# Optimization experiments

Measured on AMD Instinct MI355X. Metric: run time of the kernel, lower is better.

The kernel has to match this reference:

```python
import jax, jax.numpy as jnp
import numpy as np

B, C, S = 32768, 30, 7
COORD, NOOBJ = 5.0, 0.5


def setup_inputs() -> dict:
    key = jax.random.key(0)
    k1, k2, k3 = jax.random.split(key, 3)
    # uniform in [0.05, 1): size loss takes sqrt of raw channels, so keep them positive
    pre = jax.random.uniform(k1, (B, C, S, S), jnp.float32, 0.05, 1.0)
    lab = jax.random.uniform(k2, (B, C, S, S), jnp.float32, 0.05, 1.0)
    # channel 4 of the label is a binary objectness indicator (code tests == 1)
    objm = (jax.random.uniform(k3, (B, S, S)) < 0.3).astype(jnp.float32)
    lab = lab.at[:, 4].set(objm)
    return {"pre": pre, "lab": lab}


def _iou(b1, b2):
    # b1, b2: [B, 4, S, S] with channels (x1, y1, x2, y2); original '+1' pixel convention
    ix1 = jnp.maximum(b1[:, 0], b2[:, 0])
    iy1 = jnp.maximum(b1[:, 1], b2[:, 1])
    ix2 = jnp.minimum(b1[:, 2], b2[:, 2])
    iy2 = jnp.minimum(b1[:, 3], b2[:, 3])
    inter = jnp.maximum(ix2 - ix1 + 1.0, 0.0) * jnp.maximum(iy2 - iy1 + 1.0, 0.0)
    a1 = (b1[:, 2] - b1[:, 0] + 1.0) * (b1[:, 3] - b1[:, 1] + 1.0)
    a2 = (b2[:, 2] - b2[:, 0] + 1.0) * (b2[:, 3] - b2[:, 1] + 1.0)
    return inter / (a1 + a2 - inter)


def reference(pre, lab):
    obj = lab[:, 4] == 1.0                      # [B,S,S] objectness mask
    iou1 = _iou(pre[:, 0:4], lab[:, 0:4])       # box 1 IoU
    iou2 = _iou(pre[:, 5:9], lab[:, 5:9])       # box 2 IoU
    resp1 = iou1 >= iou2                        # box 1 responsible

    # coordinate loss: the px*64 / py*64 grid offsets cancel in (cxl - cxp)
    addr1 = COORD * ((lab[:, 0] - pre[:, 0]) ** 2 + (lab[:, 1] - pre[:, 1]) ** 2)
    addr2 = COORD * ((lab[:, 5] - pre[:, 5]) ** 2 + (lab[:, 6] - pre[:, 6]) ** 2)

    size1 = COORD * ((jnp.sqrt(pre[:, 2]) - jnp.sqrt(lab[:, 2])) ** 2
                     + (jnp.sqrt(pre[:, 3]) - jnp.sqrt(lab[:, 3])) ** 2)
    size2 = COORD * ((jnp.sqrt(pre[:, 7]) - jnp.sqrt(lab[:, 7])) ** 2
                     + (jnp.sqrt(pre[:, 8]) - jnp.sqrt(lab[:, 8])) ** 2)

    # original always uses pre[9] as the responsible confidence (faithful to source)
    conf = NOOBJ * (pre[:, 9] - jnp.where(resp1, iou1, iou2)) ** 2

    obj_terms = jnp.where(resp1, addr1 + size1, addr2 + size2) + conf
    noobj_terms = NOOBJ * (pre[:, 4] + pre[:, 9]) ** 2

    # class loss is accumulated for every cell regardless of objectness
    cls = jnp.sum((pre[:, 10:] - lab[:, 10:]) ** 2)

    total = jnp.sum(jnp.where(obj, obj_terms, noobj_terms)) + cls
    return total / B
```

## Files before the change

kernel.cpp:

```cpp
#include <hip/hip_runtime.h>


#define BATCH   32768
#define S2      49
#define CPB     1470
#define NB      2
#define GF      (NB * CPB)
#define GV      (GF / 4)
#define NGROUPS (BATCH / NB)
#define LDSB    492
#define HALF    (NB * LDSB)
#define BUFSZ   (2 * HALF)
#define NBLK    2048

__device__ __forceinline__ float iou4(float px1, float py1, float px2, float py2,
                                      float lx1, float ly1, float lx2, float ly2) {
    float ix1 = fmaxf(px1, lx1), iy1 = fmaxf(py1, ly1);
    float ix2 = fminf(px2, lx2), iy2 = fminf(py2, ly2);
    float iw = fmaxf(ix2 - ix1 + 1.0f, 0.0f);
    float ih = fmaxf(iy2 - iy1 + 1.0f, 0.0f);
    float inter = iw * ih;
    float a1 = (px2 - px1 + 1.0f) * (py2 - py1 + 1.0f);
    float a2 = (lx2 - lx1 + 1.0f) * (ly2 - ly1 + 1.0f);
    return inter / (a1 + a2 - inter);
}

__device__ __forceinline__ float cell_loss(const float* P, const float* L) {
    float p0 = P[0],   p1 = P[49],  p2 = P[98],  p3 = P[147], p4 = P[196];
    float p5 = P[245], p6 = P[294], p7 = P[343], p8 = P[392], p9 = P[441];
    float l0 = L[0],   l1 = L[49],  l2 = L[98],  l3 = L[147], l4 = L[196];
    float l5 = L[245], l6 = L[294], l7 = L[343], l8 = L[392];

    float iou1 = iou4(p0, p1, p2, p3, l0, l1, l2, l3);
    float iou2 = iou4(p5, p6, p7, p8, l5, l6, l7, l8);
    bool resp1 = iou1 >= iou2;

    float d0 = l0 - p0, d1 = l1 - p1, d5 = l5 - p5, d6 = l6 - p6;
    float addr1 = 5.0f * (d0 * d0 + d1 * d1);
    float addr2 = 5.0f * (d5 * d5 + d6 * d6);

    float e2 = sqrtf(p2) - sqrtf(l2), e3 = sqrtf(p3) - sqrtf(l3);
    float e7 = sqrtf(p7) - sqrtf(l7), e8 = sqrtf(p8) - sqrtf(l8);
    float size1 = 5.0f * (e2 * e2 + e3 * e3);
    float size2 = 5.0f * (e7 * e7 + e8 * e8);

    float du = p9 - (resp1 ? iou1 : iou2);
    float conf = 0.5f * du * du;

    float obj_terms = (resp1 ? (addr1 + size1) : (addr2 + size2)) + conf;
    float pn = p4 + p9;
    float noobj = 0.5f * pn * pn;
    return (l4 == 1.0f) ? obj_terms : noobj;
}

__device__ __forceinline__ void consume_one(float4 pv, float4 lv, int i,
                                            float* __restrict__ buf, float& acc) {
    int base = 4 * i;
    int bl = base >= CPB;
    int lo = base - bl * CPB;
    if (lo <= 486) {
        *(float4*)(buf + bl * LDSB + lo) = pv;
        *(float4*)(buf + HALF + bl * LDSB + lo) = lv;
    } else if (lo >= 490 && lo <= 1466) {
        float d0 = pv.x - lv.x, d1 = pv.y - lv.y;
        float d2 = pv.z - lv.z, d3 = pv.w - lv.w;
        acc += d0 * d0 + d1 * d1 + d2 * d2 + d3 * d3;
    } else if (lo == 488) {
        buf[bl * LDSB + 488] = pv.x;
        buf[bl * LDSB + 489] = pv.y;
        buf[HALF + bl * LDSB + 488] = lv.x;
        buf[HALF + bl * LDSB + 489] = lv.y;
        float d2 = pv.z - lv.z, d3 = pv.w - lv.w;
        acc += d2 * d2 + d3 * d3;
    } else {
        float d0 = pv.x - lv.x, d1 = pv.y - lv.y;
        acc += d0 * d0 + d1 * d1;
        buf[LDSB + 0] = pv.z;
        buf[LDSB + 1] = pv.w;
        buf[HALF + LDSB + 0] = lv.z;
        buf[HALF + LDSB + 1] = lv.w;
    }
}

__global__ __launch_bounds__(256) void yolo_loss_main(const float4* __restrict__ pre4,
                                                      const float4* __restrict__ lab4,
                                                      float* __restrict__ partials) {
    __shared__ __align__(16) float sbuf[2 * BUFSZ];
    __shared__ float red[4];
    const int tid = threadIdx.x;
    const bool t2 = tid + 512 < GV;
    float acc = 0.0f;

    float* cb   = sbuf;
    float* nbuf = sbuf + BUFSZ;

    int g = blockIdx.x;
    {
        const float4* __restrict__ ps = pre4 + (size_t)g * GV;
        const float4* __restrict__ ls = lab4 + (size_t)g * GV;
        float4 pa = ps[tid];
        float4 la = ls[tid];
        float4 pb = ps[tid + 256];
        float4 lb = ls[tid + 256];
        float4 pc, lc;
        if (t2) { pc = ps[tid + 512]; lc = ls[tid + 512]; }
        consume_one(pa, la, tid,       cb, acc);
        consume_one(pb, lb, tid + 256, cb, acc);
        if (t2) consume_one(pc, lc, tid + 512, cb, acc);
    }
    __syncthreads();

    for (;;) {
        int gn = g + gridDim.x;
        bool hn = gn < NGROUPS;
        float4 pa, la, pb, lb, pc, lc;
        if (hn) {
            const float4* __restrict__ ps = pre4 + (size_t)gn * GV;
            const float4* __restrict__ ls = lab4 + (size_t)gn * GV;
            pa = ps[tid];
            la = ls[tid];
            pb = ps[tid + 256];
            lb = ls[tid + 256];
            if (t2) { pc = ps[tid + 512]; lc = ls[tid + 512]; }
        }
        if (tid < NB * S2) {
            int bl = tid / S2, s = tid - bl * S2;
            acc += cell_loss(cb + bl * LDSB + s, cb + HALF + bl * LDSB + s);
        }
        if (hn) {
            consume_one(pa, la, tid,       nbuf, acc);
            consume_one(pb, lb, tid + 256, nbuf, acc);
            if (t2) consume_one(pc, lc, tid + 512, nbuf, acc);
        }
        __syncthreads();
        if (!hn) break;
        g = gn;
        float* t = cb; cb = nbuf; nbuf = t;
    }

    #pragma unroll
    for (int off = 32; off > 0; off >>= 1) acc += __shfl_down(acc, off);
    int lane = tid & 63, wid = tid >> 6;
    if (lane == 0) red[wid] = acc;
    __syncthreads();
    if (tid == 0) partials[blockIdx.x] = red[0] + red[1] + red[2] + red[3];
}

__global__ __launch_bounds__(256) void yolo_loss_final(const float* __restrict__ partials,
                                                       int n, float* __restrict__ out) {
    double v = 0.0;
    for (int i = (int)threadIdx.x; i < n; i += 256) v += (double)partials[i];
    __shared__ double sm[256];
    sm[threadIdx.x] = v;
    __syncthreads();
    for (int s = 128; s > 0; s >>= 1) {
        if ((int)threadIdx.x < s) sm[threadIdx.x] += sm[threadIdx.x + s];
        __syncthreads();
    }
    if (threadIdx.x == 0) out[0] = (float)(sm[0] * (1.0 / 32768.0));
}

extern "C" void kernel_launch(void* const* d_in, const int* in_sizes, int n_in,
                              void* d_out, int out_size, void* d_ws, size_t ws_size,
                              hipStream_t stream) {
    const float4* pre4 = (const float4*)d_in[0];
    const float4* lab4 = (const float4*)d_in[1];
    float* out = (float*)d_out;
    float* partials = (float*)d_ws;

    int nblk = NBLK;
    if (ws_size < (size_t)nblk * sizeof(float)) {
        nblk = (int)(ws_size / sizeof(float));
        if (nblk < 1) nblk = 1;
    }

    yolo_loss_main<<<nblk, 256, 0, stream>>>(pre4, lab4, partials);
    yolo_loss_final<<<1, 256, 0, stream>>>(partials, nblk, out);
}
```

Before: 75.86 us.

## Fuse final reduction into main kernel via last-block atomic counter

Removes the separate final-reduction launch: each block publishes its partial with a release store and bumps an atomic counter, and the last block to arrive sums all partials and writes the output. A memset of the counter is added per call. It also moves cell-loss work onto the high thread IDs (tid>=158) instead of low ones, so it lands on different wavefronts than the ones handling the extra tail loads, and it changes the block count from 2048 to 2040. This trades a kernel launch for a memset plus atomics.

Measured after the change: 260.4 us. 3.43x slower.

```diff
diff --git a/kernel.cpp b/kernel.cpp
--- a/kernel.cpp
+++ b/kernel.cpp
@@ -1,17 +1,18 @@
 #include <hip/hip_runtime.h>
 
 
-#define BATCH   32768
-#define S2      49
-#define CPB     1470
-#define NB      2
-#define GF      (NB * CPB)
-#define GV      (GF / 4)
-#define NGROUPS (BATCH / NB)
-#define LDSB    492
-#define HALF    (NB * LDSB)
-#define BUFSZ   (2 * HALF)
-#define NBLK    2048
+#define BATCH    32768
+#define S2       49
+#define CPB      1470
+#define NB       2
+#define GF       (NB * CPB)
+#define GV       (GF / 4)
+#define NGROUPS  (BATCH / NB)
+#define LDSB     492
+#define HALF     (NB * LDSB)
+#define BUFSZ    (2 * HALF)
+#define NBLK     2040
+#define CELLBASE 158
 
 __device__ __forceinline__ float iou4(float px1, float py1, float px2, float py2,
                                       float lx1, float ly1, float lx2, float ly2) {
@@ -84,9 +85,13 @@
 
 __global__ __launch_bounds__(256) void yolo_loss_main(const float4* __restrict__ pre4,
                                                       const float4* __restrict__ lab4,
-                                                      float* __restrict__ partials) {
+                                                      float* __restrict__ partials,
+                                                      unsigned int* __restrict__ ctr,
+                                                      int nblk,
+                                                      float* __restrict__ out) {
     __shared__ __align__(16) float sbuf[2 * BUFSZ];
     __shared__ float red[4];
+    __shared__ int lastflag;
     const int tid = threadIdx.x;
     const bool t2 = tid + 512 < GV;
     float acc = 0.0f;
@@ -95,47 +100,50 @@
     float* nbuf = sbuf + BUFSZ;
 
     int g = blockIdx.x;
-    {
-        const float4* __restrict__ ps = pre4 + (size_t)g * GV;
-        const float4* __restrict__ ls = lab4 + (size_t)g * GV;
-        float4 pa = ps[tid];
-        float4 la = ls[tid];
-        float4 pb = ps[tid + 256];
-        float4 lb = ls[tid + 256];
-        float4 pc, lc;
-        if (t2) { pc = ps[tid + 512]; lc = ls[tid + 512]; }
-        consume_one(pa, la, tid,       cb, acc);
-        consume_one(pb, lb, tid + 256, cb, acc);
-        if (t2) consume_one(pc, lc, tid + 512, cb, acc);
-    }
-    __syncthreads();
-
-    for (;;) {
-        int gn = g + gridDim.x;
-        bool hn = gn < NGROUPS;
-        float4 pa, la, pb, lb, pc, lc;
-        if (hn) {
-            const float4* __restrict__ ps = pre4 + (size_t)gn * GV;
-            const float4* __restrict__ ls = lab4 + (size_t)gn * GV;
-            pa = ps[tid];
-            la = ls[tid];
-            pb = ps[tid + 256];
-            lb = ls[tid + 256];
+    if (g < NGROUPS) {
+        {
+            const float4* __restrict__ ps = pre4 + (size_t)g * GV;
+            const float4* __restrict__ ls = lab4 + (size_t)g * GV;
+            float4 pa = ps[tid];
+            float4 la = ls[tid];
+            float4 pb = ps[tid + 256];
+            float4 lb = ls[tid + 256];
+            float4 pc, lc;
             if (t2) { pc = ps[tid + 512]; lc = ls[tid + 512]; }
-        }
-        if (tid < NB * S2) {
-            int bl = tid / S2, s = tid - bl * S2;
-            acc += cell_loss(cb + bl * LDSB + s, cb + HALF + bl * LDSB + s);
-        }
-        if (hn) {
-            consume_one(pa, la, tid,       nbuf, acc);
-            consume_one(pb, lb, tid + 256, nbuf, acc);
-            if (t2) consume_one(pc, lc, tid + 512, nbuf, acc);
+            consume_one(pa, la, tid,       cb, acc);
+            consume_one(pb, lb, tid + 256, cb, acc);
+            if (t2) consume_one(pc, lc, tid + 512, cb, acc);
         }
         __syncthreads();
-        if (!hn) break;
-        g = gn;
-        float* t = cb; cb = nbuf; nbuf = t;
+
+        for (;;) {
+            int gn = g + gridDim.x;
+            bool hn = gn < NGROUPS;
+            float4 pa, la, pb, lb, pc, lc;
+            if (hn) {
+                const float4* __restrict__ ps = pre4 + (size_t)gn * GV;
+                const float4* __restrict__ ls = lab4 + (size_t)gn * GV;
+                pa = ps[tid];
+                la = ls[tid];
+                pb = ps[tid + 256];
+                lb = ls[tid + 256];
+                if (t2) { pc = ps[tid + 512]; lc = ls[tid + 512]; }
+            }
+            if (tid >= CELLBASE) {
+                int ctid = tid - CELLBASE;
+                int bl = ctid / S2, s = ctid - bl * S2;
+                acc += cell_loss(cb + bl * LDSB + s, cb + HALF + bl * LDSB + s);
+            }
+            if (hn) {
+                consume_one(pa, la, tid,       nbuf, acc);
+                consume_one(pb, lb, tid + 256, nbuf, acc);
+                if (t2) consume_one(pc, lc, tid + 512, nbuf, acc);
+            }
+            __syncthreads();
+            if (!hn) break;
+            g = gn;
+            float* t = cb; cb = nbuf; nbuf = t;
+        }
     }
 
     #pragma unroll
@@ -143,21 +151,29 @@
     int lane = tid & 63, wid = tid >> 6;
     if (lane == 0) red[wid] = acc;
     __syncthreads();
-    if (tid == 0) partials[blockIdx.x] = red[0] + red[1] + red[2] + red[3];
-}
+    if (tid == 0) {
+        float bs = red[0] + red[1] + red[2] + red[3];
+        __hip_atomic_store(&partials[blockIdx.x], bs, __ATOMIC_RELEASE,
+                           __HIP_MEMORY_SCOPE_AGENT);
+        unsigned prev = __hip_atomic_fetch_add(ctr, 1u, __ATOMIC_ACQ_REL,
+                                               __HIP_MEMORY_SCOPE_AGENT);
+        lastflag = (prev == (unsigned)(nblk - 1)) ? 1 : 0;
+    }
+    __syncthreads();
 
-__global__ __launch_bounds__(256) void yolo_loss_final(const float* __restrict__ partials,
-                                                       int n, float* __restrict__ out) {
-    double v = 0.0;
-    for (int i = (int)threadIdx.x; i < n; i += 256) v += (double)partials[i];
-    __shared__ double sm[256];
-    sm[threadIdx.x] = v;
-    __syncthreads();
-    for (int s = 128; s > 0; s >>= 1) {
-        if ((int)threadIdx.x < s) sm[threadIdx.x] += sm[threadIdx.x + s];
+    if (lastflag) {
+        double v = 0.0;
+        for (int i = tid; i < nblk; i += 256)
+            v += (double)__hip_atomic_load(&partials[i], __ATOMIC_RELAXED,
+                                           __HIP_MEMORY_SCOPE_AGENT);
+        #pragma unroll
+        for (int off = 32; off > 0; off >>= 1) v += __shfl_down(v, off);
+        __shared__ double dred[4];
+        if ((tid & 63) == 0) dred[tid >> 6] = v;
         __syncthreads();
+        if (tid == 0)
+            out[0] = (float)((dred[0] + dred[1] + dred[2] + dred[3]) * (1.0 / 32768.0));
     }
-    if (threadIdx.x == 0) out[0] = (float)(sm[0] * (1.0 / 32768.0));
 }
 
 extern "C" void kernel_launch(void* const* d_in, const int* in_sizes, int n_in,
@@ -166,14 +182,16 @@
     const float4* pre4 = (const float4*)d_in[0];
     const float4* lab4 = (const float4*)d_in[1];
     float* out = (float*)d_out;
-    float* partials = (float*)d_ws;
+    unsigned int* ctr = (unsigned int*)d_ws;
+    float* partials = (float*)d_ws + 1;
 
     int nblk = NBLK;
-    if (ws_size < (size_t)nblk * sizeof(float)) {
-        nblk = (int)(ws_size / sizeof(float));
+    size_t need = (size_t)(nblk + 1) * sizeof(float);
+    if (ws_size < need) {
+        nblk = (int)(ws_size / sizeof(float)) - 1;
         if (nblk < 1) nblk = 1;
     }
 
-    yolo_loss_main<<<nblk, 256, 0, stream>>>(pre4, lab4, partials);
-    yolo_loss_final<<<1, 256, 0, stream>>>(partials, nblk, out);
+    hipMemsetAsync(d_ws, 0, sizeof(unsigned int), stream);
+    yolo_loss_main<<<nblk, 256, 0, stream>>>(pre4, lab4, partials, ctr, nblk, out);
 }
```

## Skip loading unused label channel 9 and drop LDS double buffering

Applied to the files above, without the earlier changes.

Each batch element's label channel 9 is never read by the loss, so the float4 label loads covering that range (offsets 441-486 within each element) are now skipped, along with the LDS writes for label data that is never consumed. At the same time the software-pipelined double buffer, which prefetched the next group while computing the current one, is replaced by a simple single-buffer loop with two barriers per group. This is meant to cut global read traffic and halve LDS use, which may raise occupancy. The cost is that loads are no longer explicitly overlapped with compute inside a block, and the kernel now relies on multiple resident blocks per CU to hide memory latency.

Result: faster. 74.16 us (-2.2%).

```diff
diff --git a/kernel.cpp b/kernel.cpp
--- a/kernel.cpp
+++ b/kernel.cpp
@@ -53,14 +53,16 @@
     return (l4 == 1.0f) ? obj_terms : noobj;
 }
 
-__device__ __forceinline__ void consume_one(float4 pv, float4 lv, int i,
-                                            float* __restrict__ buf, float& acc) {
+__device__ __forceinline__ void consume_pair(float4 pv, float4 lv, int i,
+                                             bool lab_ok,
+                                             float* __restrict__ buf, float& acc) {
     int base = 4 * i;
     int bl = base >= CPB;
     int lo = base - bl * CPB;
     if (lo <= 486) {
         *(float4*)(buf + bl * LDSB + lo) = pv;
-        *(float4*)(buf + HALF + bl * LDSB + lo) = lv;
+        if (lab_ok)
+            *(float4*)(buf + HALF + bl * LDSB + lo) = lv;
     } else if (lo >= 490 && lo <= 1466) {
         float d0 = pv.x - lv.x, d1 = pv.y - lv.y;
         float d2 = pv.z - lv.z, d3 = pv.w - lv.w;
@@ -68,8 +70,6 @@
     } else if (lo == 488) {
         buf[bl * LDSB + 488] = pv.x;
         buf[bl * LDSB + 489] = pv.y;
-        buf[HALF + bl * LDSB + 488] = lv.x;
-        buf[HALF + bl * LDSB + 489] = lv.y;
         float d2 = pv.z - lv.z, d3 = pv.w - lv.w;
         acc += d2 * d2 + d3 * d3;
     } else {
@@ -82,60 +82,48 @@
     }
 }
 
+__device__ __forceinline__ bool lab_needed(int i) {
+    int base = 4 * i;
+    int bl = base >= CPB;
+    int lo = base - bl * CPB;
+    return !(lo >= 441 && lo <= 486);
+}
+
 __global__ __launch_bounds__(256) void yolo_loss_main(const float4* __restrict__ pre4,
                                                       const float4* __restrict__ lab4,
                                                       float* __restrict__ partials) {
-    __shared__ __align__(16) float sbuf[2 * BUFSZ];
+    __shared__ __align__(16) float sbuf[BUFSZ];
     __shared__ float red[4];
     const int tid = threadIdx.x;
-    const bool t2 = tid + 512 < GV;
+    const int i0 = tid, i1 = tid + 256, i2 = tid + 512;
+    const bool t2 = i2 < GV;
+    const bool nl0 = lab_needed(i0);
+    const bool nl1 = lab_needed(i1);
+    const bool nl2 = t2 ? lab_needed(i2) : false;
     float acc = 0.0f;
 
-    float* cb   = sbuf;
-    float* nbuf = sbuf + BUFSZ;
-
-    int g = blockIdx.x;
-    {
+    for (int g = blockIdx.x; g < NGROUPS; g += gridDim.x) {
         const float4* __restrict__ ps = pre4 + (size_t)g * GV;
         const float4* __restrict__ ls = lab4 + (size_t)g * GV;
-        float4 pa = ps[tid];
-        float4 la = ls[tid];
-        float4 pb = ps[tid + 256];
-        float4 lb = ls[tid + 256];
-        float4 pc, lc;
-        if (t2) { pc = ps[tid + 512]; lc = ls[tid + 512]; }
-        consume_one(pa, la, tid,       cb, acc);
-        consume_one(pb, lb, tid + 256, cb, acc);
-        if (t2) consume_one(pc, lc, tid + 512, cb, acc);
-    }
-    __syncthreads();
+        float4 pa = ps[i0];
+        float4 pb = ps[i1];
+        float4 pc;
+        if (t2) pc = ps[i2];
+        float4 la, lb, lc;
+        if (nl0) la = ls[i0];
+        if (nl1) lb = ls[i1];
+        if (nl2) lc = ls[i2];
 
-    for (;;) {
-        int gn = g + gridDim.x;
-        bool hn = gn < NGROUPS;
-        float4 pa, la, pb, lb, pc, lc;
-        if (hn) {
-            const float4* __restrict__ ps = pre4 + (size_t)gn * GV;
-            const float4* __restrict__ ls = lab4 + (size_t)gn * GV;
-            pa = ps[tid];
-            la = ls[tid];
-            pb = ps[tid + 256];
-            lb = ls[tid + 256];
-            if (t2) { pc = ps[tid + 512]; lc = ls[tid + 512]; }
-        }
+        consume_pair(pa, la, i0, nl0, sbuf, acc);
+        consume_pair(pb, lb, i1, nl1, sbuf, acc);
+        if (t2) consume_pair(pc, lc, i2, nl2, sbuf, acc);
+        __syncthreads();
+
         if (tid < NB * S2) {
             int bl = tid / S2, s = tid - bl * S2;
-            acc += cell_loss(cb + bl * LDSB + s, cb + HALF + bl * LDSB + s);
-        }
-        if (hn) {
-            consume_one(pa, la, tid,       nbuf, acc);
-            consume_one(pb, lb, tid + 256, nbuf, acc);
-            if (t2) consume_one(pc, lc, tid + 512, nbuf, acc);
+            acc += cell_loss(sbuf + bl * LDSB + s, sbuf + HALF + bl * LDSB + s);
         }
         __syncthreads();
-        if (!hn) break;
-        g = gn;
-        float* t = cb; cb = nbuf; nbuf = t;
     }
 
     #pragma unroll
```
